# Optimization experiments

Hardware: AMD Instinct MI355X
Metric: run time of the kernel (lower is better)

## Reference

```python
import jax, jax.numpy as jnp
import numpy as np

N_POINTS = 4096
N_PROJS = 2000


def setup_inputs() -> dict:
    key = jax.random.key(0)
    k1, k2, k3 = jax.random.split(key, 3)
    Xs = jax.random.normal(k1, (N_POINTS, 3), dtype=jnp.float32)
    Xt = jax.random.normal(k2, (N_POINTS, 3), dtype=jnp.float32)
    Us = jax.random.normal(k3, (N_PROJS, 3, 2), dtype=jnp.float32)
    return {"Xs": Xs, "Xt": Xt, "Us": Us}


def _project_to_circle(X, Us):
    # X: [n, d], Us: [P, d, 2] -> angles in [0, 1): [P, n]
    Xp = jnp.einsum('pdk,nd->pnk', Us, X)  # [P, n, 2]
    nrm = jnp.sqrt(jnp.sum(Xp * Xp, axis=-1, keepdims=True))
    Xp = Xp / jnp.maximum(nrm, 1e-12)  # F.normalize
    return (jnp.arctan2(-Xp[..., 1], -Xp[..., 0]) + np.pi) / (2 * np.pi)


def _emd1d_circle_p1(u_values, v_values):
    # Circular W1 via level-median (Delon et al.). u,v: [P, n], [P, m]
    P, n = u_values.shape
    m = v_values.shape[-1]
    dt = u_values.dtype
    u_w = jnp.full((P, n), 1.0 / n, dtype=dt)
    v_w = jnp.full((P, m), 1.0 / m, dtype=dt)
    us = jnp.sort(u_values, axis=-1)
    vs = jnp.sort(v_values, axis=-1)
    vals = jnp.concatenate([us, vs], axis=-1)            # [P, n+m]
    sorter = jnp.argsort(vals, axis=-1)
    vals_sorted = jnp.take_along_axis(vals, sorter, axis=-1)
    w_cat = jnp.concatenate([u_w, -v_w], axis=-1)
    cdf_diff = jnp.cumsum(jnp.take_along_axis(w_cat, sorter, axis=-1), axis=-1)
    cdf_sorter = jnp.argsort(cdf_diff, axis=-1)
    cdf_diff_sorted = jnp.take_along_axis(cdf_diff, cdf_sorter, axis=-1)
    vals_pad = jnp.concatenate([vals_sorted, jnp.ones((P, 1), dtype=dt)], axis=-1)
    delta = vals_pad[..., 1:] - vals_pad[..., :-1]
    weight_sorted = jnp.take_along_axis(delta, cdf_sorter, axis=-1)
    sum_weights = jnp.cumsum(weight_sorted, axis=-1) - 0.5
    sum_weights = jnp.where(sum_weights < 0, jnp.inf, sum_weights)
    inds = jnp.argmin(sum_weights, axis=-1)
    levMed = jnp.take_along_axis(cdf_diff_sorted, inds[:, None], axis=-1)  # [P, 1]
    return jnp.sum(delta * jnp.abs(cdf_diff - levMed), axis=-1)  # [P]


def reference(Xs, Xt, Us):
    Xps = _project_to_circle(Xs, Us)  # [P, n]
    Xpt = _project_to_circle(Xt, Us)  # [P, m]
    w1 = _emd1d_circle_p1(Xps, Xpt)
    return jnp.mean(w1)
```

## Files before the change

### kernel.cpp

```cpp
#include <hip/hip_runtime.h>
#include <math.h>

#define NPTS   4096
#define NPROJ  2000
#define NB     512
#define NMERGE 8192
#define VPT    16

__device__ __forceinline__ int sw(int i) {
    return (i & ~31) | ((i + (i >> 5)) & 31);
}

__device__ __forceinline__ void local_merge(float v[VPT], bool asc) {
    #pragma unroll
    for (int j = 8; j >= 1; j >>= 1) {
        #pragma unroll
        for (int e = 0; e < VPT; ++e) {
            if ((e & j) == 0) {
                float a = v[e], b = v[e | j];
                float mn = fminf(a, b), mx = fmaxf(a, b);
                v[e]     = asc ? mn : mx;
                v[e | j] = asc ? mx : mn;
            }
        }
    }
}

__global__ __launch_bounds__(NB) void swd_kernel(
    const float* __restrict__ Xs, const float* __restrict__ Xt,
    const float* __restrict__ Us, float* __restrict__ out)
{
    __shared__ float keys[NMERGE];

    const int tid  = threadIdx.x;
    const int arr  = tid >> 8;
    const int c    = tid & 255;
    const int lane = tid & 63;
    const int wid  = tid >> 6;
    const int p    = blockIdx.x;

    const float u00 = Us[p*6+0], u01 = Us[p*6+1];
    const float u10 = Us[p*6+2], u11 = Us[p*6+3];
    const float u20 = Us[p*6+4], u21 = Us[p*6+5];

    const float pi_f   = 3.14159265358979323846f;
    const float inv2pi = 0.15915494309189535f;

    const float* __restrict__ X = arr ? Xt : Xs;

    float v[VPT];
    {
        const float4* X4 = (const float4*)(X + c * (VPT * 3));
        #pragma unroll
        for (int t = 0; t < 4; ++t) {
            float4 q0 = X4[t*3+0], q1 = X4[t*3+1], q2 = X4[t*3+2];
            #define ANG(x,y,z) ((atan2f(-((x)*u01+(y)*u11+(z)*u21), \
                                        -((x)*u00+(y)*u10+(z)*u20)) + pi_f) * inv2pi)
            v[t*4+0] = ANG(q0.x, q0.y, q0.z);
            v[t*4+1] = ANG(q0.w, q1.x, q1.y);
            v[t*4+2] = ANG(q1.z, q1.w, q2.x);
            v[t*4+3] = ANG(q2.y, q2.z, q2.w);
            #undef ANG
        }
    }

    #pragma unroll
    for (int k = 2; k <= 8; k <<= 1) {
        #pragma unroll
        for (int j = k >> 1; j >= 1; j >>= 1) {
            #pragma unroll
            for (int e = 0; e < VPT; ++e) {
                if ((e & j) == 0) {
                    bool asc = ((e & k) == 0);
                    float a = v[e], b = v[e | j];
                    float mn = fminf(a, b), mx = fmaxf(a, b);
                    v[e]     = asc ? mn : mx;
                    v[e | j] = asc ? mx : mn;
                }
            }
        }
    }

    local_merge(v, (c & 1) == 0);

    #pragma unroll
    for (int k = 32; k <= 1024; k <<= 1) {
        bool asc = ((c & (k >> 4)) == 0);
        #pragma unroll
        for (int d = k >> 5; d >= 1; d >>= 1) {
            bool keepmin = (((c & d) == 0) == asc);
            #pragma unroll
            for (int e = 0; e < VPT; ++e) {
                float o = __shfl_xor(v[e], d, 64);
                v[e] = keepmin ? fminf(v[e], o) : fmaxf(v[e], o);
            }
        }
        local_merge(v, asc);
    }

    #define LDS_XCHG(PXOR, KEEPMIN_EXPR)                                   \
    {                                                                      \
        _Pragma("unroll")                                                  \
        for (int e = 0; e < VPT; ++e) keys[sw(tid * VPT + e)] = v[e];      \
        __syncthreads();                                                   \
        const int pbase = (tid ^ (PXOR)) * VPT;                            \
        const bool keepmin = (KEEPMIN_EXPR);                               \
        _Pragma("unroll")                                                  \
        for (int e = 0; e < VPT; ++e) {                                    \
            float o = keys[sw(pbase + e)];                                 \
            v[e] = keepmin ? fminf(v[e], o) : fmaxf(v[e], o);              \
        }                                                                  \
        __syncthreads();                                                   \
    }

    {
        bool asc = ((c & 128) == 0);
        LDS_XCHG(64, ((c & 64) == 0) == asc);
        #pragma unroll
        for (int d = 32; d >= 1; d >>= 1) {
            bool keepmin = (((c & d) == 0) == asc);
            #pragma unroll
            for (int e = 0; e < VPT; ++e) {
                float o = __shfl_xor(v[e], d, 64);
                v[e] = keepmin ? fminf(v[e], o) : fmaxf(v[e], o);
            }
        }
        local_merge(v, asc);
    }

    LDS_XCHG(128, (c & 128) == 0);
    LDS_XCHG(64,  (c & 64) == 0);
    #pragma unroll
    for (int d = 32; d >= 1; d >>= 1) {
        bool keepmin = ((c & d) == 0);
        #pragma unroll
        for (int e = 0; e < VPT; ++e) {
            float o = __shfl_xor(v[e], d, 64);
            v[e] = keepmin ? fminf(v[e], o) : fmaxf(v[e], o);
        }
    }
    local_merge(v, true);
    #undef LDS_XCHG

    #pragma unroll
    for (int e = 0; e < VPT; ++e) keys[sw(tid * VPT + e)] = v[e];
    __syncthreads();

    int c_init;
    int offmin = 32, offmax = -32;
    unsigned int c8[4] = {0,0,0,0};
    {
        const int d0 = tid * VPT;
        int lo = d0 > NPTS ? d0 - NPTS : 0;
        int hi = d0 < NPTS ? d0 : NPTS;
        while (lo < hi) {
            int mid = (lo + hi) >> 1;
            if (keys[sw(mid)] <= keys[sw(NPTS + (d0 - 1 - mid))]) lo = mid + 1; else hi = mid;
        }
        int i = lo, j = d0 - lo;
        c_init = i - j;
        const float FMAXV = 3.402823466e+38f;
        float cu = (i < NPTS) ? keys[sw(i)] : FMAXV;
        float cv = (j < NPTS) ? keys[sw(NPTS + j)] : FMAXV;
        #pragma unroll
        for (int s = 0; s < VPT; ++s) {
            float cur;
            if (cu <= cv) { cur = cu; ++i; cu = (i < NPTS) ? keys[sw(i)] : FMAXV; }
            else          { cur = cv; ++j; cv = (j < NPTS) ? keys[sw(NPTS + j)] : FMAXV; }
            float nxt = fminf(cu, cv);
            if (nxt == FMAXV) nxt = 1.0f;
            v[s] = nxt - cur;
            int off = (i - j) - c_init;
            offmin = min(offmin, off);
            offmax = max(offmax, off);
            c8[s >> 2] |= ((unsigned int)(off & 0xff)) << ((s & 3) * 8);
        }
    }

    __syncthreads();
    int*   ired = (int*)keys;
    float* red  = keys + 16;

    int cmn = c_init + offmin, cmx = c_init + offmax;
    #pragma unroll
    for (int o = 32; o >= 1; o >>= 1) {
        cmn = min(cmn, __shfl_xor(cmn, o, 64));
        cmx = max(cmx, __shfl_xor(cmx, o, 64));
    }
    if (lane == 0) { ired[wid] = cmn; ired[8 + wid] = cmx; }
    __syncthreads();
    {
        int a0 = min(min(ired[0], ired[1]), min(ired[2], ired[3]));
        int a1 = min(min(ired[4], ired[5]), min(ired[6], ired[7]));
        cmn = min(a0, a1);
        int b0 = max(max(ired[8], ired[9]),  max(ired[10], ired[11]));
        int b1 = max(max(ired[12], ired[13]), max(ired[14], ired[15]));
        cmx = max(b0, b1);
    }

    int lo_c = cmn - 1, hi_c = cmx;
    int it = 0;
    #pragma unroll 1
    while (hi_c - lo_c > 1) {
        const int mid = (lo_c + hi_c) >> 1;
        const int thr = mid - c_init;
        float s_loc = 0.0f;
        #pragma unroll
        for (int s = 0; s < VPT; ++s) {
            int off = (int)(c8[s >> 2] << ((3 - (s & 3)) * 8)) >> 24;
            s_loc += (off <= thr) ? v[s] : 0.0f;
        }
        #pragma unroll
        for (int o = 32; o >= 1; o >>= 1) s_loc += __shfl_down(s_loc, o, 64);
        if (lane == 0) red[it * 8 + wid] = s_loc;
        __syncthreads();
        float S = 0.0f;
        #pragma unroll
        for (int w = 0; w < 8; ++w) S += red[it * 8 + w];
        if (S >= 0.5f) hi_c = mid; else lo_c = mid;
        ++it;
    }
    const int cstar = hi_c;

    float part = 0.0f;
    {
        const int thr = cstar - c_init;
        #pragma unroll
        for (int s = 0; s < VPT; ++s) {
            int off = (int)(c8[s >> 2] << ((3 - (s & 3)) * 8)) >> 24;
            part += v[s] * fabsf((float)(off - thr));
        }
    }
    #pragma unroll
    for (int o = 32; o >= 1; o >>= 1) part += __shfl_down(part, o, 64);
    if (lane == 0) red[15 * 8 + wid] = part;
    __syncthreads();
    if (tid == 0) {
        float w1 = 0.0f;
        #pragma unroll
        for (int w = 0; w < 8; ++w) w1 += red[15 * 8 + w];
        w1 *= (1.0f / 4096.0f);
        atomicAdd(out, w1 * (1.0f / (float)NPROJ));
    }
}

extern "C" void kernel_launch(void* const* d_in, const int* in_sizes, int n_in,
                              void* d_out, int out_size, void* d_ws, size_t ws_size,
                              hipStream_t stream) {
    const float* Xs = (const float*)d_in[0];
    const float* Xt = (const float*)d_in[1];
    const float* Us = (const float*)d_in[2];
    float* out = (float*)d_out;

    hipMemsetAsync(out, 0, sizeof(float), stream);
    swd_kernel<<<NPROJ, NB, 0, stream>>>(Xs, Xt, Us, out);
}
```

Before: 230.1 us.

## Replace level-median binary search with histogram prefix-sum closed form

Drops the iterative binary search over CDF levels, which needed one block-wide reduction and barrier per step, plus the final weighted-absolute-deviation pass. Instead, gap weights are binned into a shared-memory histogram by CDF level with atomicAdd. A block-wide prefix scan follows, and W1 is computed in closed form as the sum of min(T, G-T) over the cumulative totals. This swaps roughly log(range) barrier rounds for LDS atomics and a chunked scan whose cost grows with the level range. It also relies on the median identity, which changes the float summation order.

```diff
diff --git a/kernel.cpp b/kernel.cpp
--- a/kernel.cpp
+++ b/kernel.cpp
@@ -178,8 +178,8 @@
     }
 
     __syncthreads();
-    int*   ired = (int*)keys;
-    float* red  = keys + 16;
+    int*   ired = (int*)(keys + 4104);
+    float* red  = keys + 4120;
 
     int cmn = c_init + offmin, cmx = c_init + offmax;
     #pragma unroll
@@ -197,48 +197,62 @@
         int b1 = max(max(ired[12], ired[13]), max(ired[14], ired[15]));
         cmx = max(b0, b1);
     }
-
-    int lo_c = cmn - 1, hi_c = cmx;
-    int it = 0;
-    #pragma unroll 1
-    while (hi_c - lo_c > 1) {
-        const int mid = (lo_c + hi_c) >> 1;
-        const int thr = mid - c_init;
-        float s_loc = 0.0f;
+    const int R = cmx - cmn + 1;
+
+    for (int b = tid; b < R; b += NB) keys[b] = 0.0f;
+    __syncthreads();
+    {
+        const int base = c_init - cmn;
         #pragma unroll
         for (int s = 0; s < VPT; ++s) {
             int off = (int)(c8[s >> 2] << ((3 - (s & 3)) * 8)) >> 24;
-            s_loc += (off <= thr) ? v[s] : 0.0f;
-        }
-        #pragma unroll
-        for (int o = 32; o >= 1; o >>= 1) s_loc += __shfl_down(s_loc, o, 64);
-        if (lane == 0) red[it * 8 + wid] = s_loc;
+            atomicAdd(&keys[base + off], v[s]);
+        }
+    }
+    __syncthreads();
+
+    const int nch = (R + NB - 1) / NB;
+    float carry = 0.0f;
+    for (int ch = 0; ch < nch; ++ch) {
+        const int idx = ch * NB + tid;
+        float x = (idx < R) ? keys[idx] : 0.0f;
+        #pragma unroll
+        for (int o = 1; o <= 32; o <<= 1) {
+            float t = __shfl_up(x, o, 64);
+            if (lane >= o) x += t;
+        }
+        if (lane == 63) red[wid] = x;
         __syncthreads();
-        float S = 0.0f;
-        #pragma unroll
-        for (int w = 0; w < 8; ++w) S += red[it * 8 + w];
-        if (S >= 0.5f) hi_c = mid; else lo_c = mid;
-        ++it;
-    }
-    const int cstar = hi_c;
-
-    float part = 0.0f;
-    {
-        const int thr = cstar - c_init;
-        #pragma unroll
-        for (int s = 0; s < VPT; ++s) {
-            int off = (int)(c8[s >> 2] << ((3 - (s & 3)) * 8)) >> 24;
-            part += v[s] * fabsf((float)(off - thr));
-        }
-    }
-    #pragma unroll
-    for (int o = 32; o >= 1; o >>= 1) part += __shfl_down(part, o, 64);
-    if (lane == 0) red[15 * 8 + wid] = part;
+        float prefix = carry, ctot = 0.0f;
+        #pragma unroll
+        for (int w = 0; w < 8; ++w) {
+            float rw = red[w];
+            prefix += (w < wid) ? rw : 0.0f;
+            ctot   += rw;
+        }
+        x += prefix;
+        if (idx < R) keys[idx] = x;
+        carry += ctot;
+        __syncthreads();
+    }
+    const float G = carry;
+
+    float f = 0.0f;
+    for (int ch = 0; ch < nch; ++ch) {
+        const int idx = ch * NB + tid;
+        if (idx < R - 1) {
+            float T = keys[idx];
+            f += (T < 0.5f) ? T : (G - T);
+        }
+    }
+    #pragma unroll
+    for (int o = 32; o >= 1; o >>= 1) f += __shfl_down(f, o, 64);
+    if (lane == 0) red[wid] = f;
     __syncthreads();
     if (tid == 0) {
         float w1 = 0.0f;
         #pragma unroll
-        for (int w = 0; w < 8; ++w) w1 += red[15 * 8 + w];
+        for (int w = 0; w < 8; ++w) w1 += red[w];
         w1 *= (1.0f / 4096.0f);
         atomicAdd(out, w1 * (1.0f / (float)NPROJ));
     }
```

New measurement: 304.2 us. +32.2%, slower.
